# Performance work log

Measured on AMD Instinct MI355X. Metric: run time of the kernel, lower is better.

Reference implementation:

```python
import jax, jax.numpy as jnp
import numpy as np

N_QUBITS = 10
DIM = 2 ** N_QUBITS
N_TOKENS = 32
LAYERS = 2
DEGREE = 3
VOCAB = 32000
EMB = 512
N_PARAMS = 4 * N_QUBITS * LAYERS      # angles per token circuit
N_PARAMS_FF = 4 * N_QUBITS            # quantum feedforward (1 layer)
BATCH = 32


def _ry(state, wire, theta, n):
    # state: [B, 2**n] complex64; theta: [B] float32. RY = [[c,-s],[s,c]], c=cos(th/2)
    st = state.reshape(-1, 2 ** wire, 2, 2 ** (n - wire - 1))
    c = jnp.cos(theta / 2)[:, None, None]
    s = jnp.sin(theta / 2)[:, None, None]
    a, b = st[:, :, 0, :], st[:, :, 1, :]
    st = jnp.stack([c * a - s * b, s * a + c * b], axis=2)
    return st.reshape(-1, 2 ** n)


def _crx(state, ctrl, tgt, theta, n):
    # controlled-RX: apply RX=[[c,-i s],[-i s,c]] on tgt where ctrl bit == 1
    lo, hi = (ctrl, tgt) if ctrl < tgt else (tgt, ctrl)
    st = state.reshape(-1, 2 ** lo, 2, 2 ** (hi - lo - 1), 2, 2 ** (n - hi - 1))
    caxis = 2 if ctrl < tgt else 4
    taxis = 4 if ctrl < tgt else 2
    c = jnp.cos(theta / 2).reshape(-1, 1, 1, 1, 1, 1)
    s = jnp.sin(theta / 2).reshape(-1, 1, 1, 1, 1, 1)
    c0 = jax.lax.index_in_dim(st, 0, caxis, keepdims=True)
    c1 = jax.lax.index_in_dim(st, 1, caxis, keepdims=True)
    a = jax.lax.index_in_dim(c1, 0, taxis, keepdims=True)
    b = jax.lax.index_in_dim(c1, 1, taxis, keepdims=True)
    na = c * a - 1j * s * b
    nb = -1j * s * a + c * b
    c1 = jnp.concatenate([na, nb], axis=taxis)
    st = jnp.concatenate([c0, c1], axis=caxis)
    return st.reshape(-1, 2 ** n)


def _ansatz14(state, params, n, layers):
    # gate order of ansatz 14 (arXiv:1905.10876); params: [B, 4*n*layers]
    idx = 0
    for _ in range(layers):
        for i in range(n):
            state = _ry(state, i, params[:, idx], n); idx += 1
        for i in range(n - 1, -1, -1):
            state = _crx(state, i, (i + 1) % n, params[:, idx], n); idx += 1
        for i in range(n):
            state = _ry(state, i, params[:, idx], n); idx += 1
        for i in [n - 1] + list(range(n - 1)):
            state = _crx(state, i, (i - 1) % n, params[:, idx], n); idx += 1
    return state


def _measure_xyz(state, n):
    # expectation of X,Y,Z on every wire; output [B, 3*n] ordered [x..., y..., z...]
    B = state.shape[0]
    xs, ys, zs = [], [], []
    for w in range(n):
        st = state.reshape(B, 2 ** w, 2, 2 ** (n - w - 1))
        a, b = st[:, :, 0, :], st[:, :, 1, :]
        z = jnp.sum(jnp.conj(a) * b, axis=(1, 2))
        xs.append(2.0 * jnp.real(z))
        ys.append(2.0 * jnp.imag(z))
        zs.append(jnp.sum(jnp.real(a * jnp.conj(a)) - jnp.real(b * jnp.conj(b)), axis=(1, 2)))
    return jnp.stack(xs + ys + zs, axis=1)


def _forward(x, emb, w_ang, b_ang, qsvt_coeffs, lcu_re, lcu_im, qff_params, w1, b1, w2, b2):
    B, T = x.shape
    lcu = (lcu_re + 1j * lcu_im).astype(jnp.complex64)
    lcu = lcu / jnp.maximum(jnp.sum(jnp.abs(lcu)), 1e-12)          # p=1 normalize
    angles = (emb[x] @ w_ang.T + b_ang).reshape(B * T, N_PARAMS)   # [B*T, P]
    init = jnp.zeros((B, DIM), jnp.complex64).at[:, 0].set(1.0)
    acc = qsvt_coeffs[0] * init
    mono = init
    for k in range(1, DEGREE + 1):
        rep = jnp.repeat(mono, T, axis=0)                          # [B*T, D]
        st = _ansatz14(rep, angles, N_QUBITS, LAYERS).reshape(B, T, DIM)
        mono = jnp.einsum('bwi,w->bi', st, lcu)                    # LCU combine
        acc = acc + qsvt_coeffs[k] * mono
    qsvt_state = acc / jnp.sum(jnp.abs(qsvt_coeffs))
    norm = jnp.linalg.norm(qsvt_state, axis=-1, keepdims=True)
    normed = qsvt_state / jnp.maximum(norm, 1e-12)
    qff = jnp.broadcast_to(qff_params[None, :], (B, N_PARAMS_FF))
    st2 = _ansatz14(normed, qff, N_QUBITS, 1)
    ev = _measure_xyz(st2, N_QUBITS)                               # [B, 3*nq]
    h = jax.nn.relu(ev @ w1.T + b1)
    logits = h @ w2.T + b2
    return logits, jnp.mean(norm[:, 0])


def setup_inputs() -> dict:
    key = jax.random.key(0)
    ks = jax.random.split(key, 9)
    return {
        'x': jax.random.randint(ks[0], (BATCH, N_TOKENS), 0, VOCAB, dtype=jnp.int32),
        'emb': jax.random.normal(ks[1], (VOCAB, EMB), jnp.float32) * 0.02,
        'w_ang': jax.random.normal(ks[2], (N_PARAMS, EMB), jnp.float32) * (1.0 / np.sqrt(EMB)),
        'b_ang': jnp.zeros((N_PARAMS,), jnp.float32),
        'qsvt_coeffs': jax.random.uniform(ks[3], (DEGREE + 1,), jnp.float32),
        'lcu_re': jax.random.uniform(ks[4], (N_TOKENS,), jnp.float32),
        'lcu_im': jax.random.uniform(ks[5], (N_TOKENS,), jnp.float32),
        'qff_params': jax.random.uniform(ks[6], (N_PARAMS_FF,), jnp.float32),
        'w1': jax.random.normal(ks[7], (EMB, 3 * N_QUBITS), jnp.float32) * (1.0 / np.sqrt(3 * N_QUBITS)),
        'b1': jnp.zeros((EMB,), jnp.float32),
        'w2': jax.random.normal(ks[8], (VOCAB, EMB), jnp.float32) * (1.0 / np.sqrt(EMB)),
        'b2': jnp.zeros((VOCAB,), jnp.float32),
    }


def reference(x, emb, w_ang, b_ang, qsvt_coeffs, lcu_re, lcu_im, qff_params, w1, b1, w2, b2):
    return _forward(x, emb, w_ang, b_ang, qsvt_coeffs, lcu_re, lcu_im, qff_params, w1, b1, w2, b2)
```

## Files before the change

kernel.cpp:

```cpp
#include <hip/hip_runtime.h>
#include <math.h>

#define DEV __device__ __forceinline__

namespace {

struct C2 { float x, y; };

constexpr size_t OFF_CS   = 0;
constexpr size_t OFF_NRM  = 163988;
constexpr size_t OFF_MONO = 164096;
constexpr size_t OFF_ACC  = 229632;
constexpr size_t OFF_ST   = 295168;
constexpr size_t OFF_H    = 2393280;


template<int P>
DEV void ry_gate(C2 v[16], int lane, float c, float s) {
  if constexpr (P >= 6) {
    constexpr int rm = 1 << (P - 6);
#pragma unroll
    for (int r = 0; r < 16; ++r) {
      if ((r & rm) == 0) {
        C2 a = v[r], b = v[r | rm];
        v[r].x      = fmaf(c, a.x, -s * b.x);
        v[r].y      = fmaf(c, a.y, -s * b.y);
        v[r | rm].x = fmaf(s, a.x,  c * b.x);
        v[r | rm].y = fmaf(s, a.y,  c * b.y);
      }
    }
  } else {
    constexpr int lm = 1 << P;
    float sg = (lane & lm) ? s : -s;
#pragma unroll
    for (int r = 0; r < 16; ++r) {
      float px = __shfl_xor(v[r].x, lm, 64);
      float py = __shfl_xor(v[r].y, lm, 64);
      v[r].x = fmaf(c, v[r].x, sg * px);
      v[r].y = fmaf(c, v[r].y, sg * py);
    }
  }
}

template<int PC, int PT>
DEV void crx_gate(C2 v[16], int lane, float c, float s) {
  if constexpr (PT >= 6) {
    constexpr int tm = 1 << (PT - 6);
#pragma unroll
    for (int r = 0; r < 16; ++r) {
      if ((r & tm) == 0) {
        if constexpr (PC >= 6) {
          constexpr int cm = 1 << (PC - 6);
          if ((r & cm) != 0) {
            C2 a = v[r], b = v[r | tm];
            v[r].x      = fmaf(c, a.x,  s * b.y);
            v[r].y      = fmaf(c, a.y, -s * b.x);
            v[r | tm].x = fmaf(c, b.x,  s * a.y);
            v[r | tm].y = fmaf(c, b.y, -s * a.x);
          }
        } else {
          constexpr int cl = 1 << PC;
          bool ct = (lane & cl) != 0;
          C2 a = v[r], b = v[r | tm];
          float nax = fmaf(c, a.x,  s * b.y);
          float nay = fmaf(c, a.y, -s * b.x);
          float nbx = fmaf(c, b.x,  s * a.y);
          float nby = fmaf(c, b.y, -s * a.x);
          v[r].x      = ct ? nax : a.x;
          v[r].y      = ct ? nay : a.y;
          v[r | tm].x = ct ? nbx : b.x;
          v[r | tm].y = ct ? nby : b.y;
        }
      }
    }
  } else {
    constexpr int tm = 1 << PT;
#pragma unroll
    for (int r = 0; r < 16; ++r) {
      if constexpr (PC >= 6) {
        constexpr int cm = 1 << (PC - 6);
        if ((r & cm) == 0) continue;
      }
      float px = __shfl_xor(v[r].x, tm, 64);
      float py = __shfl_xor(v[r].y, tm, 64);
      float nx = fmaf(c, v[r].x,  s * py);
      float ny = fmaf(c, v[r].y, -s * px);
      if constexpr (PC >= 6) {
        v[r].x = nx; v[r].y = ny;
      } else {
        constexpr int cl = 1 << PC;
        bool ct = (lane & cl) != 0;
        v[r].x = ct ? nx : v[r].x;
        v[r].y = ct ? ny : v[r].y;
      }
    }
  }
}

#define RYG(w, g)       ry_gate<9-(w)>(v, lane, cs[2*(g)], cs[2*(g)+1])
#define CRXG(cw, tw, g) crx_gate<9-(cw), 9-(tw)>(v, lane, cs[2*(g)], cs[2*(g)+1])

DEV void apply_layer(C2 v[16], int lane, const float* __restrict__ cs) {
  RYG(0,0); RYG(1,1); RYG(2,2); RYG(3,3); RYG(4,4);
  RYG(5,5); RYG(6,6); RYG(7,7); RYG(8,8); RYG(9,9);
  CRXG(9,0,10); CRXG(8,9,11); CRXG(7,8,12); CRXG(6,7,13); CRXG(5,6,14);
  CRXG(4,5,15); CRXG(3,4,16); CRXG(2,3,17); CRXG(1,2,18); CRXG(0,1,19);
  RYG(0,20); RYG(1,21); RYG(2,22); RYG(3,23); RYG(4,24);
  RYG(5,25); RYG(6,26); RYG(7,27); RYG(8,28); RYG(9,29);
  CRXG(9,8,30); CRXG(0,9,31); CRXG(1,0,32); CRXG(2,1,33); CRXG(3,2,34);
  CRXG(4,3,35); CRXG(5,4,36); CRXG(6,5,37); CRXG(7,6,38); CRXG(8,7,39);
}

template<int P>
DEV void measure_wire(const C2 v[16], int lane, float* ev, int w) {
  float x = 0.f, y = 0.f, z = 0.f;
  if constexpr (P >= 6) {
    constexpr int rm = 1 << (P - 6);
#pragma unroll
    for (int r = 0; r < 16; ++r) {
      if ((r & rm) == 0) {
        C2 a = v[r], b = v[r | rm];
        x += a.x*b.x + a.y*b.y;
        y += a.x*b.y - a.y*b.x;
        z += (a.x*a.x + a.y*a.y) - (b.x*b.x + b.y*b.y);
      }
    }
  } else {
    constexpr int lm = 1 << P;
#pragma unroll
    for (int r = 0; r < 16; ++r) {
      float px = __shfl_xor(v[r].x, lm, 64);
      float py = __shfl_xor(v[r].y, lm, 64);
      if ((lane & lm) == 0) {
        C2 a = v[r];
        x += a.x*px + a.y*py;
        y += a.x*py - a.y*px;
        z += (a.x*a.x + a.y*a.y) - (px*px + py*py);
      }
    }
  }
  for (int s = 1; s < 64; s <<= 1) {
    x += __shfl_xor(x, s, 64);
    y += __shfl_xor(y, s, 64);
    z += __shfl_xor(z, s, 64);
  }
  if (lane == 0) {
    ev[w]      = 2.f * x;
    ev[10 + w] = 2.f * y;
    ev[20 + w] = z;
  }
}

DEV void measure_all(const C2 v[16], int lane, float* ev) {
  measure_wire<9>(v, lane, ev, 0);
  measure_wire<8>(v, lane, ev, 1);
  measure_wire<7>(v, lane, ev, 2);
  measure_wire<6>(v, lane, ev, 3);
  measure_wire<5>(v, lane, ev, 4);
  measure_wire<4>(v, lane, ev, 5);
  measure_wire<3>(v, lane, ev, 6);
  measure_wire<2>(v, lane, ev, 7);
  measure_wire<1>(v, lane, ev, 8);
  measure_wire<0>(v, lane, ev, 9);
}


__global__ __launch_bounds__(128) void k_angles(const int* __restrict__ x,
                                                const float* __restrict__ emb,
                                                const float* __restrict__ w_ang,
                                                const float* __restrict__ b_ang,
                                                float* __restrict__ ws) {
  __shared__ float4 e2[2][128];
  int g = blockIdx.x;
  int tid = threadIdx.x;
  int r0 = x[2 * g], r1 = x[2 * g + 1];
  e2[0][tid] = ((const float4*)(emb + (size_t)r0 * 512))[tid];
  e2[1][tid] = ((const float4*)(emb + (size_t)r1 * 512))[tid];
  __syncthreads();
  if (tid < 80) {
    const float4* wr = (const float4*)(w_ang + (size_t)tid * 512);
    float bv = b_ang[tid];
    float a0 = bv, a1 = bv;
#pragma unroll 4
    for (int j = 0; j < 128; ++j) {
      float4 w = wr[j];
      float4 e0 = e2[0][j], e1 = e2[1][j];
      a0 = fmaf(w.x, e0.x, a0); a0 = fmaf(w.y, e0.y, a0);
      a0 = fmaf(w.z, e0.z, a0); a0 = fmaf(w.w, e0.w, a0);
      a1 = fmaf(w.x, e1.x, a1); a1 = fmaf(w.y, e1.y, a1);
      a1 = fmaf(w.z, e1.z, a1); a1 = fmaf(w.w, e1.w, a1);
    }
    float t0 = 0.5f * a0, t1 = 0.5f * a1;
    ws[OFF_CS + (size_t)(2 * g) * 160 + 2 * tid]         = cosf(t0);
    ws[OFF_CS + (size_t)(2 * g) * 160 + 2 * tid + 1]     = sinf(t0);
    ws[OFF_CS + (size_t)(2 * g + 1) * 160 + 2 * tid]     = cosf(t1);
    ws[OFF_CS + (size_t)(2 * g + 1) * 160 + 2 * tid + 1] = sinf(t1);
  }
}

__global__ __launch_bounds__(256) void k_evolve(float* __restrict__ ws,
                                                const float* __restrict__ lr,
                                                const float* __restrict__ li,
                                                int k) {
  __shared__ float cs_lds[640];
  int tid = threadIdx.x;
  const float* csg = ws + OFF_CS + (size_t)blockIdx.x * 640;
  for (int i = tid; i < 640; i += 256) cs_lds[i] = csg[i];
  __syncthreads();
  int wid = tid >> 6, lane = tid & 63;
  int state = blockIdx.x * 4 + wid;
  int b = state >> 5, t = state & 31;

  float lre_v = 0.f, lim_v = 0.f;
  if (lane < 32) { lre_v = lr[lane]; lim_v = li[lane]; }
  float ab = sqrtf(lre_v * lre_v + lim_v * lim_v);
  for (int s = 1; s < 64; s <<= 1) ab += __shfl_xor(ab, s, 64);
  float invL = 1.f / fmaxf(ab, 1e-12f);
  float wre = __shfl(lre_v, t, 64) * invL;
  float wim = __shfl(lim_v, t, 64) * invL;

  C2 v[16];
  if (k == 1) {
#pragma unroll
    for (int r = 0; r < 16; ++r) {
      v[r].x = (r == 0 && lane == 0) ? 1.f : 0.f;
      v[r].y = 0.f;
    }
  } else {
    const float2* mono = (const float2*)(ws + OFF_MONO) + (size_t)b * 1024;
#pragma unroll
    for (int r = 0; r < 16; ++r) {
      float2 m = mono[(r << 6) | lane];
      v[r].x = m.x; v[r].y = m.y;
    }
  }
  const float* csw = &cs_lds[wid * 160];
  apply_layer(v, lane, csw);
  apply_layer(v, lane, csw + 80);
  float2* st = (float2*)(ws + OFF_ST) + (size_t)state * 1024;
#pragma unroll
  for (int r = 0; r < 16; ++r) {
    st[(r << 6) | lane] = make_float2(wre * v[r].x - wim * v[r].y,
                                      wre * v[r].y + wim * v[r].x);
  }
}

__global__ void k_reduce(float* __restrict__ ws, const float* __restrict__ coef, int k) {
  int idx = blockIdx.x * 256 + threadIdx.x;
  int b = idx >> 10, i = idx & 1023;
  const float2* st = (const float2*)(ws + OFF_ST) + (size_t)b * 32768 + i;
  float sx = 0.f, sy = 0.f;
#pragma unroll
  for (int t = 0; t < 32; ++t) {
    float2 vv = st[t * 1024];
    sx += vv.x; sy += vv.y;
  }
  float2* mono = (float2*)(ws + OFF_MONO);
  float2* acc  = (float2*)(ws + OFF_ACC);
  float ck = coef[k];
  if (k == 1) {
    float e0 = (i == 0) ? coef[0] : 0.f;
    acc[idx] = make_float2(fmaf(ck, sx, e0), ck * sy);
    mono[idx] = make_float2(sx, sy);
  } else {
    float2 a = acc[idx];
    a.x = fmaf(ck, sx, a.x);
    a.y = fmaf(ck, sy, a.y);
    acc[idx] = a;
    if (k < 3) mono[idx] = make_float2(sx, sy);
  }
}

__global__ __launch_bounds__(256) void k_final(float* __restrict__ ws,
                                               const float* __restrict__ coef,
                                               const float* __restrict__ qff,
                                               const float* __restrict__ w1,
                                               const float* __restrict__ b1) {
  __shared__ float qff_lds[80];
  __shared__ float ev_lds[30];
  int tid = threadIdx.x;
  int b = blockIdx.x;
  if (tid < 40) {
    float th = 0.5f * qff[tid];
    qff_lds[2 * tid]     = cosf(th);
    qff_lds[2 * tid + 1] = sinf(th);
  }
  __syncthreads();
  if (tid < 64) {
    int lane = tid;
    float den = fabsf(coef[0]) + fabsf(coef[1]) + fabsf(coef[2]) + fabsf(coef[3]);
    float invd = 1.f / den;
    const float2* accp = (const float2*)(ws + OFF_ACC) + (size_t)b * 1024;
    C2 v[16];
    float ssum = 0.f;
#pragma unroll
    for (int r = 0; r < 16; ++r) {
      float2 m = accp[(r << 6) | lane];
      v[r].x = m.x * invd; v[r].y = m.y * invd;
      ssum += v[r].x * v[r].x + v[r].y * v[r].y;
    }
    for (int s = 1; s < 64; s <<= 1) ssum += __shfl_xor(ssum, s, 64);
    float nrm = sqrtf(ssum);
    if (lane == 0) ws[OFF_NRM + b] = nrm;
    float sc = 1.f / fmaxf(nrm, 1e-12f);
#pragma unroll
    for (int r = 0; r < 16; ++r) { v[r].x *= sc; v[r].y *= sc; }
    apply_layer(v, lane, qff_lds);
    measure_all(v, lane, ev_lds);
  }
  __syncthreads();
#pragma unroll
  for (int jj = 0; jj < 2; ++jj) {
    int j = tid + jj * 256;
    const float* wr = w1 + (size_t)j * 30;
    float a = b1[j];
#pragma unroll
    for (int q = 0; q < 30; ++q) a = fmaf(ev_lds[q], wr[q], a);
    ws[OFF_H + b * 512 + j] = fmaxf(a, 0.f);
  }
}

__global__ __launch_bounds__(256) void k_logits(const float* __restrict__ ws,
                                                const float* __restrict__ w2,
                                                const float* __restrict__ b2,
                                                float* __restrict__ out) {
  __shared__ float4 hT[4096];
  int tid = threadIdx.x;
  if (blockIdx.x == 0 && tid == 0) {
    float s = 0.f;
    for (int i = 0; i < 32; ++i) s += ws[OFF_NRM + i];
    out[32000u * 32u] = s * (1.f / 32.f);
  }
  const float4* hg = (const float4*)(ws + OFF_H);
#pragma unroll
  for (int p = 0; p < 16; ++p) {
    int idx = tid + p * 256;
    int m = idx >> 7, kf4 = idx & 127;
    hT[m * 128 + (kf4 ^ (m >> 3))] = hg[idx];
  }
  __syncthreads();

  int wv = tid >> 6, lane = tid & 63;
  int mg = lane & 3, nl = lane >> 2;
  int nbase = blockIdx.x * 128;
  float acc[8][8];
#pragma unroll
  for (int j = 0; j < 8; ++j)
#pragma unroll
    for (int mi = 0; mi < 8; ++mi) acc[j][mi] = 0.f;

  const float* wbase = w2 + (size_t)(nbase + nl * 8) * 512 + wv * 128;
  int kqb = wv * 32;
  for (int kf4 = 0; kf4 < 32; ++kf4) {
    int kcol = kqb + kf4;
    float4 h4[8];
#pragma unroll
    for (int mi = 0; mi < 8; ++mi) {
      int m = mg * 8 + mi;
      h4[mi] = hT[m * 128 + (kcol ^ mg)];
    }
#pragma unroll
    for (int j = 0; j < 8; ++j) {
      float4 w4 = *(const float4*)(wbase + (size_t)j * 512 + kf4 * 4);
#pragma unroll
      for (int mi = 0; mi < 8; ++mi) {
        acc[j][mi] = fmaf(w4.x, h4[mi].x, acc[j][mi]);
        acc[j][mi] = fmaf(w4.y, h4[mi].y, acc[j][mi]);
        acc[j][mi] = fmaf(w4.z, h4[mi].z, acc[j][mi]);
        acc[j][mi] = fmaf(w4.w, h4[mi].w, acc[j][mi]);
      }
    }
  }

  __syncthreads();
  if (wv != 0) {
    int r = wv - 1;
    float4* cb = hT + r * 1024 + lane * 16;
#pragma unroll
    for (int mi = 0; mi < 8; ++mi) {
#pragma unroll
      for (int jh = 0; jh < 2; ++jh) {
        int q = mi * 2 + jh;
        float4 vv = make_float4(acc[jh*4+0][mi], acc[jh*4+1][mi],
                                acc[jh*4+2][mi], acc[jh*4+3][mi]);
        cb[q ^ (lane & 15)] = vv;
      }
    }
  }
  __syncthreads();
  if (wv == 0) {
#pragma unroll
    for (int r = 0; r < 3; ++r) {
      const float4* cb = hT + r * 1024 + lane * 16;
#pragma unroll
      for (int mi = 0; mi < 8; ++mi) {
#pragma unroll
        for (int jh = 0; jh < 2; ++jh) {
          int q = mi * 2 + jh;
          float4 vv = cb[q ^ (lane & 15)];
          acc[jh*4+0][mi] += vv.x;
          acc[jh*4+1][mi] += vv.y;
          acc[jh*4+2][mi] += vv.z;
          acc[jh*4+3][mi] += vv.w;
        }
      }
    }
    float4 b2lo = *(const float4*)(b2 + nbase + nl * 8);
    float4 b2hi = *(const float4*)(b2 + nbase + nl * 8 + 4);
#pragma unroll
    for (int mi = 0; mi < 8; ++mi) {
      int m = mg * 8 + mi;
      float* orow = out + (size_t)m * 32000 + nbase + nl * 8;
      float4 lo = make_float4(acc[0][mi] + b2lo.x, acc[1][mi] + b2lo.y,
                              acc[2][mi] + b2lo.z, acc[3][mi] + b2lo.w);
      float4 hi = make_float4(acc[4][mi] + b2hi.x, acc[5][mi] + b2hi.y,
                              acc[6][mi] + b2hi.z, acc[7][mi] + b2hi.w);
      *(float4*)(orow)     = lo;
      *(float4*)(orow + 4) = hi;
    }
  }
}

}

extern "C" void kernel_launch(void* const* d_in, const int* in_sizes, int n_in,
                              void* d_out, int out_size, void* d_ws, size_t ws_size,
                              hipStream_t stream) {
  (void)in_sizes; (void)n_in; (void)out_size; (void)ws_size;
  const int*   x    = (const int*)d_in[0];
  const float* emb  = (const float*)d_in[1];
  const float* wang = (const float*)d_in[2];
  const float* bang = (const float*)d_in[3];
  const float* coef = (const float*)d_in[4];
  const float* lre  = (const float*)d_in[5];
  const float* lim  = (const float*)d_in[6];
  const float* qff  = (const float*)d_in[7];
  const float* w1   = (const float*)d_in[8];
  const float* b1   = (const float*)d_in[9];
  const float* w2   = (const float*)d_in[10];
  const float* b2   = (const float*)d_in[11];
  float* out = (float*)d_out;
  float* ws  = (float*)d_ws;

  hipLaunchKernelGGL(k_angles, dim3(512), dim3(128), 0, stream, x, emb, wang, bang, ws);
  for (int k = 1; k <= 3; ++k) {
    hipLaunchKernelGGL(k_evolve, dim3(256), dim3(256), 0, stream, ws, lre, lim, k);
    hipLaunchKernelGGL(k_reduce, dim3(128), dim3(256), 0, stream, ws, coef, k);
  }
  hipLaunchKernelGGL(k_final,  dim3(32),  dim3(256), 0, stream, ws, coef, qff, w1, b1);
  hipLaunchKernelGGL(k_logits, dim3(250), dim3(256), 0, stream, ws, w2, b2, out);
}
```

Before: 164.0 us.

## Fuse final reduce into k_final, retile logits and batch angle rows

Drops the third k_reduce launch. k_final now sums the 32 token states itself and adds the degree-3 term into LDS before normalising. The logits GEMM uses 64-column tiles over 500 blocks, with a simpler all-wave LDS reduction of the K-split partials, to spread work over more CUs. k_angles handles four tokens per block so each w_ang row load is reused across more dot products. The trade-offs are that k_final runs on only 32 blocks yet now does the large reduction, and the logits kernel issues more blocks that each reload the whole activation tile.

```diff
diff --git a/kernel.cpp b/kernel.cpp
--- a/kernel.cpp
+++ b/kernel.cpp
@@ -170,31 +170,38 @@
                                                 const float* __restrict__ w_ang,
                                                 const float* __restrict__ b_ang,
                                                 float* __restrict__ ws) {
-  __shared__ float4 e2[2][128];
+  __shared__ float4 e4[4][128];
   int g = blockIdx.x;
   int tid = threadIdx.x;
-  int r0 = x[2 * g], r1 = x[2 * g + 1];
-  e2[0][tid] = ((const float4*)(emb + (size_t)r0 * 512))[tid];
-  e2[1][tid] = ((const float4*)(emb + (size_t)r1 * 512))[tid];
+#pragma unroll
+  for (int rr = 0; rr < 4; ++rr) {
+    int row = x[4 * g + rr];
+    e4[rr][tid] = ((const float4*)(emb + (size_t)row * 512))[tid];
+  }
   __syncthreads();
   if (tid < 80) {
     const float4* wr = (const float4*)(w_ang + (size_t)tid * 512);
     float bv = b_ang[tid];
-    float a0 = bv, a1 = bv;
+    float a0 = bv, a1 = bv, a2 = bv, a3 = bv;
 #pragma unroll 4
     for (int j = 0; j < 128; ++j) {
       float4 w = wr[j];
-      float4 e0 = e2[0][j], e1 = e2[1][j];
+      float4 e0 = e4[0][j], e1 = e4[1][j], e2 = e4[2][j], e3 = e4[3][j];
       a0 = fmaf(w.x, e0.x, a0); a0 = fmaf(w.y, e0.y, a0);
       a0 = fmaf(w.z, e0.z, a0); a0 = fmaf(w.w, e0.w, a0);
       a1 = fmaf(w.x, e1.x, a1); a1 = fmaf(w.y, e1.y, a1);
       a1 = fmaf(w.z, e1.z, a1); a1 = fmaf(w.w, e1.w, a1);
-    }
-    float t0 = 0.5f * a0, t1 = 0.5f * a1;
-    ws[OFF_CS + (size_t)(2 * g) * 160 + 2 * tid]         = cosf(t0);
-    ws[OFF_CS + (size_t)(2 * g) * 160 + 2 * tid + 1]     = sinf(t0);
-    ws[OFF_CS + (size_t)(2 * g + 1) * 160 + 2 * tid]     = cosf(t1);
-    ws[OFF_CS + (size_t)(2 * g + 1) * 160 + 2 * tid + 1] = sinf(t1);
+      a2 = fmaf(w.x, e2.x, a2); a2 = fmaf(w.y, e2.y, a2);
+      a2 = fmaf(w.z, e2.z, a2); a2 = fmaf(w.w, e2.w, a2);
+      a3 = fmaf(w.x, e3.x, a3); a3 = fmaf(w.y, e3.y, a3);
+      a3 = fmaf(w.z, e3.z, a3); a3 = fmaf(w.w, e3.w, a3);
+    }
+    float t0 = 0.5f * a0, t1 = 0.5f * a1, t2 = 0.5f * a2, t3 = 0.5f * a3;
+    size_t base = OFF_CS + (size_t)(4 * g) * 160 + 2 * tid;
+    ws[base]           = cosf(t0); ws[base + 1]       = sinf(t0);
+    ws[base + 160]     = cosf(t1); ws[base + 161]     = sinf(t1);
+    ws[base + 320]     = cosf(t2); ws[base + 321]     = sinf(t2);
+    ws[base + 480]     = cosf(t3); ws[base + 481]     = sinf(t3);
   }
 }
 
@@ -267,7 +274,7 @@
     a.x = fmaf(ck, sx, a.x);
     a.y = fmaf(ck, sy, a.y);
     acc[idx] = a;
-    if (k < 3) mono[idx] = make_float2(sx, sy);
+    mono[idx] = make_float2(sx, sy);
   }
 }
 
@@ -277,6 +284,7 @@
                                                const float* __restrict__ w1,
                                                const float* __restrict__ b1) {
   __shared__ float qff_lds[80];
+  __shared__ float2 sv[1024];
   __shared__ float ev_lds[30];
   int tid = threadIdx.x;
   int b = blockIdx.x;
@@ -285,18 +293,32 @@
     qff_lds[2 * tid]     = cosf(th);
     qff_lds[2 * tid + 1] = sinf(th);
   }
+  float den = fabsf(coef[0]) + fabsf(coef[1]) + fabsf(coef[2]) + fabsf(coef[3]);
+  float invd = 1.f / den;
+  float c3 = coef[3];
+  const float2* stb  = (const float2*)(ws + OFF_ST) + (size_t)b * 32768;
+  const float2* accb = (const float2*)(ws + OFF_ACC) + (size_t)b * 1024;
+#pragma unroll
+  for (int q = 0; q < 4; ++q) {
+    int i = tid + q * 256;
+    float sx = 0.f, sy = 0.f;
+#pragma unroll
+    for (int t = 0; t < 32; ++t) {
+      float2 vv = stb[t * 1024 + i];
+      sx += vv.x; sy += vv.y;
+    }
+    float2 a = accb[i];
+    sv[i] = make_float2(fmaf(c3, sx, a.x) * invd, fmaf(c3, sy, a.y) * invd);
+  }
   __syncthreads();
   if (tid < 64) {
     int lane = tid;
-    float den = fabsf(coef[0]) + fabsf(coef[1]) + fabsf(coef[2]) + fabsf(coef[3]);
-    float invd = 1.f / den;
-    const float2* accp = (const float2*)(ws + OFF_ACC) + (size_t)b * 1024;
     C2 v[16];
     float ssum = 0.f;
 #pragma unroll
     for (int r = 0; r < 16; ++r) {
-      float2 m = accp[(r << 6) | lane];
-      v[r].x = m.x * invd; v[r].y = m.y * invd;
+      float2 m = sv[(r << 6) | lane];
+      v[r].x = m.x; v[r].y = m.y;
       ssum += v[r].x * v[r].x + v[r].y * v[r].y;
     }
     for (int s = 1; s < 64; s <<= 1) ssum += __shfl_xor(ssum, s, 64);
@@ -342,15 +364,16 @@
 
   int wv = tid >> 6, lane = tid & 63;
   int mg = lane & 3, nl = lane >> 2;
-  int nbase = blockIdx.x * 128;
-  float acc[8][8];
-#pragma unroll
-  for (int j = 0; j < 8; ++j)
+  int nbase = blockIdx.x * 64;
+  float acc[4][8];
+#pragma unroll
+  for (int j = 0; j < 4; ++j)
 #pragma unroll
     for (int mi = 0; mi < 8; ++mi) acc[j][mi] = 0.f;
 
-  const float* wbase = w2 + (size_t)(nbase + nl * 8) * 512 + wv * 128;
+  const float* wbase = w2 + (size_t)(nbase + nl * 4) * 512 + wv * 128;
   int kqb = wv * 32;
+#pragma unroll 2
   for (int kf4 = 0; kf4 < 32; ++kf4) {
     int kcol = kqb + kf4;
     float4 h4[8];
@@ -360,7 +383,7 @@
       h4[mi] = hT[m * 128 + (kcol ^ mg)];
     }
 #pragma unroll
-    for (int j = 0; j < 8; ++j) {
+    for (int j = 0; j < 4; ++j) {
       float4 w4 = *(const float4*)(wbase + (size_t)j * 512 + kf4 * 4);
 #pragma unroll
       for (int mi = 0; mi < 8; ++mi) {
@@ -373,50 +396,31 @@
   }
 
   __syncthreads();
-  if (wv != 0) {
-    int r = wv - 1;
-    float4* cb = hT + r * 1024 + lane * 16;
-#pragma unroll
-    for (int mi = 0; mi < 8; ++mi) {
-#pragma unroll
-      for (int jh = 0; jh < 2; ++jh) {
-        int q = mi * 2 + jh;
-        float4 vv = make_float4(acc[jh*4+0][mi], acc[jh*4+1][mi],
-                                acc[jh*4+2][mi], acc[jh*4+3][mi]);
-        cb[q ^ (lane & 15)] = vv;
-      }
-    }
-  }
-  __syncthreads();
-  if (wv == 0) {
-#pragma unroll
-    for (int r = 0; r < 3; ++r) {
-      const float4* cb = hT + r * 1024 + lane * 16;
-#pragma unroll
-      for (int mi = 0; mi < 8; ++mi) {
-#pragma unroll
-        for (int jh = 0; jh < 2; ++jh) {
-          int q = mi * 2 + jh;
-          float4 vv = cb[q ^ (lane & 15)];
-          acc[jh*4+0][mi] += vv.x;
-          acc[jh*4+1][mi] += vv.y;
-          acc[jh*4+2][mi] += vv.z;
-          acc[jh*4+3][mi] += vv.w;
-        }
-      }
-    }
-    float4 b2lo = *(const float4*)(b2 + nbase + nl * 8);
-    float4 b2hi = *(const float4*)(b2 + nbase + nl * 8 + 4);
-#pragma unroll
-    for (int mi = 0; mi < 8; ++mi) {
-      int m = mg * 8 + mi;
-      float* orow = out + (size_t)m * 32000 + nbase + nl * 8;
-      float4 lo = make_float4(acc[0][mi] + b2lo.x, acc[1][mi] + b2lo.y,
-                              acc[2][mi] + b2lo.z, acc[3][mi] + b2lo.w);
-      float4 hi = make_float4(acc[4][mi] + b2hi.x, acc[5][mi] + b2hi.y,
-                              acc[6][mi] + b2hi.z, acc[7][mi] + b2hi.w);
-      *(float4*)(orow)     = lo;
-      *(float4*)(orow + 4) = hi;
+#pragma unroll
+  for (int mi = 0; mi < 8; ++mi) {
+    hT[wv * 512 + lane * 8 + (mi ^ (lane & 7))] =
+        make_float4(acc[0][mi], acc[1][mi], acc[2][mi], acc[3][mi]);
+  }
+  __syncthreads();
+  {
+    int lane2 = tid & 63, grp = tid >> 6;
+    int mg2 = lane2 & 3, nl2 = lane2 >> 2;
+#pragma unroll
+    for (int jj = 0; jj < 2; ++jj) {
+      int mi2 = grp * 2 + jj;
+      float4 s0 = hT[0 * 512 + lane2 * 8 + (mi2 ^ (lane2 & 7))];
+      float4 s1 = hT[1 * 512 + lane2 * 8 + (mi2 ^ (lane2 & 7))];
+      float4 s2 = hT[2 * 512 + lane2 * 8 + (mi2 ^ (lane2 & 7))];
+      float4 s3 = hT[3 * 512 + lane2 * 8 + (mi2 ^ (lane2 & 7))];
+      float sx = s0.x + s1.x + s2.x + s3.x;
+      float sy = s0.y + s1.y + s2.y + s3.y;
+      float sz = s0.z + s1.z + s2.z + s3.z;
+      float sw = s0.w + s1.w + s2.w + s3.w;
+      int m = mg2 * 8 + mi2;
+      int col = nbase + nl2 * 4;
+      float4 b2v = *(const float4*)(b2 + col);
+      float4 res = make_float4(sx + b2v.x, sy + b2v.y, sz + b2v.z, sw + b2v.w);
+      *(float4*)(out + (size_t)m * 32000 + col) = res;
     }
   }
 }
@@ -442,11 +446,12 @@
   float* out = (float*)d_out;
   float* ws  = (float*)d_ws;
 
-  hipLaunchKernelGGL(k_angles, dim3(512), dim3(128), 0, stream, x, emb, wang, bang, ws);
-  for (int k = 1; k <= 3; ++k) {
-    hipLaunchKernelGGL(k_evolve, dim3(256), dim3(256), 0, stream, ws, lre, lim, k);
-    hipLaunchKernelGGL(k_reduce, dim3(128), dim3(256), 0, stream, ws, coef, k);
-  }
+  hipLaunchKernelGGL(k_angles, dim3(256), dim3(128), 0, stream, x, emb, wang, bang, ws);
+  hipLaunchKernelGGL(k_evolve, dim3(256), dim3(256), 0, stream, ws, lre, lim, 1);
+  hipLaunchKernelGGL(k_reduce, dim3(128), dim3(256), 0, stream, ws, coef, 1);
+  hipLaunchKernelGGL(k_evolve, dim3(256), dim3(256), 0, stream, ws, lre, lim, 2);
+  hipLaunchKernelGGL(k_reduce, dim3(128), dim3(256), 0, stream, ws, coef, 2);
+  hipLaunchKernelGGL(k_evolve, dim3(256), dim3(256), 0, stream, ws, lre, lim, 3);
   hipLaunchKernelGGL(k_final,  dim3(32),  dim3(256), 0, stream, ws, coef, qff, w1, b1);
-  hipLaunchKernelGGL(k_logits, dim3(250), dim3(256), 0, stream, ws, w2, b2, out);
-}
+  hipLaunchKernelGGL(k_logits, dim3(500), dim3(256), 0, stream, ws, w2, b2, out);
+}
```

Result: no change. 165.4 us (+0.9%).
